# Optimization experiments

Hardware: AMD Instinct MI355X
Metric: run time of the kernel (lower is better)

The kernel has to match this reference:

```python
import jax, jax.numpy as jnp
import numpy as np

B, S, DIN, DOUT, R, E = 4, 4096, 2048, 2048, 16, 12
MULTIPLIER = 1.0
SCALE = 16.0 / 16.0  # alpha / lora_dim


def setup_inputs() -> dict:
    key = jax.random.key(0)
    k_x, k_g, k_org, k_dn, k_up = jax.random.split(key, 5)
    x = jax.random.normal(k_x, (B, S, DIN), dtype=jnp.float32)
    # router gate over experts (external router output; softmax-normalized)
    gate = jax.nn.softmax(jax.random.normal(k_g, (B, E), dtype=jnp.float32), axis=-1)
    W_org = jax.random.normal(k_org, (DOUT, DIN), dtype=jnp.float32) * (1.0 / np.sqrt(DIN))
    W_down = jax.random.normal(k_dn, (R, DIN), dtype=jnp.float32) * (1.0 / np.sqrt(DIN))
    W_up = jax.random.normal(k_up, (E, DOUT, R), dtype=jnp.float32) * 0.02
    return {"x": x, "gate": gate, "W_org": W_org, "W_down": W_down, "W_up": W_up}


def reference(x, gate, W_org, W_down, W_up):
    # Frozen base linear (no bias)
    org = jnp.einsum('bsi,oi->bso', x, W_org)
    # Shared down-projection to rank R
    lx = jnp.einsum('bsi,ri->bsr', x, W_down)                 # [B,S,R]
    # Gate-weighted combination of expert up-projections
    combined = jnp.einsum('be,eor->bor', gate, W_up)          # [B,DOUT,R]
    # Batched low-rank up-projection (torch bmm(lx, combined^T))
    out = jnp.einsum('bsr,bor->bso', lx, combined)            # [B,S,DOUT]
    return org + out * (MULTIPLIER * SCALE)
```

## Files before the change

### kernel.cpp

```cpp
#include <hip/hip_runtime.h>
#include <cstdint>
#include <cstddef>

#define B_    4
#define S_    4096
#define DIN_  2048
#define DOUT_ 2048
#define R_    16
#define E_    12

typedef __bf16 bf16x8  __attribute__((ext_vector_type(8)));
typedef float  floatx4  __attribute__((ext_vector_type(4)));
typedef float  floatx16 __attribute__((ext_vector_type(16)));

__device__ __forceinline__ unsigned int f2bf(float f) {
  unsigned int u = __builtin_bit_cast(unsigned int, f);
  u += 0x7fffu + ((u >> 16) & 1u);
  return u >> 16;
}

__device__ __forceinline__ void async_copy16(const void* g, void* l) {
  __builtin_amdgcn_global_load_lds(
      (const __attribute__((address_space(1))) void*)g,
      (__attribute__((address_space(3))) void*)l,
      16, 0, 0);
}

__global__ __launch_bounds__(256) void cvt_x_kernel(const float* __restrict__ x,
                                                    unsigned short* __restrict__ xb) {
  size_t idx = ((size_t)blockIdx.x * 256 + threadIdx.x) * 8;
  float4 a = *(const float4*)(x + idx);
  float4 b = *(const float4*)(x + idx + 4);
  uint4 o;
  o.x = f2bf(a.x) | (f2bf(a.y) << 16);
  o.y = f2bf(a.z) | (f2bf(a.w) << 16);
  o.z = f2bf(b.x) | (f2bf(b.y) << 16);
  o.w = f2bf(b.z) | (f2bf(b.w) << 16);
  *(uint4*)(xb + idx) = o;
}

__global__ __launch_bounds__(256) void prep_misc_kernel(const float* __restrict__ W_org,
                                                        const float* __restrict__ W_down,
                                                        const float* __restrict__ gate,
                                                        const float* __restrict__ W_up,
                                                        unsigned short* __restrict__ worg,
                                                        unsigned short* __restrict__ wdb,
                                                        unsigned short* __restrict__ cmb) {
  const int bid = blockIdx.x;
  const int tid = threadIdx.x;
  if (bid < 2064) {
    const float* src;
    unsigned short* dst;
    size_t idx;
    if (bid < 2048) { src = W_org;  dst = worg; idx = ((size_t)bid * 256 + tid) * 8; }
    else            { src = W_down; dst = wdb;  idx = ((size_t)(bid - 2048) * 256 + tid) * 8; }
    float4 a = *(const float4*)(src + idx);
    float4 b = *(const float4*)(src + idx + 4);
    uint4 o;
    o.x = f2bf(a.x) | (f2bf(a.y) << 16);
    o.y = f2bf(a.z) | (f2bf(a.w) << 16);
    o.z = f2bf(b.x) | (f2bf(b.y) << 16);
    o.w = f2bf(b.z) | (f2bf(b.w) << 16);
    *(uint4*)(dst + idx) = o;
  } else {
    const int idx = (bid - 2064) * 256 + tid;
    const int b   = idx >> 15;
    const int orr = idx & 32767;
    float s = 0.f;
#pragma unroll
    for (int e = 0; e < E_; ++e)
      s += gate[b * E_ + e] * W_up[(size_t)e * DOUT_ * R_ + orr];
    cmb[idx] = (unsigned short)f2bf(s);
  }
}

__global__ __launch_bounds__(256) void lx_kernel(const unsigned short* __restrict__ xb,
                                                 const unsigned short* __restrict__ wdb,
                                                 unsigned short* __restrict__ lxb) {
  const int tid  = threadIdx.x;
  const int lane = tid & 63;
  const int wave = tid >> 6;
  const int grp  = wave >> 1;
  const int kh   = wave & 1;
  const int q    = lane >> 4;
  const int mrow = lane & 15;
  const int row0 = blockIdx.x * 32 + grp * 16;

  floatx4 acc = {};
  const unsigned short* aptr = xb  + (size_t)(row0 + mrow) * DIN_ + kh * 1024 + q * 8;
  const unsigned short* bptr = wdb + (size_t)mrow * DIN_ + kh * 1024 + q * 8;
#pragma unroll 4
  for (int ks = 0; ks < 32; ++ks) {
    bf16x8 av = *(const bf16x8*)(aptr + ks * 32);
    bf16x8 bv = *(const bf16x8*)(bptr + ks * 32);
    acc = __builtin_amdgcn_mfma_f32_16x16x32_bf16(av, bv, acc, 0, 0, 0);
  }

  __shared__ float red[2][64 * 4];
  if (kh == 1) *(floatx4*)&red[grp][lane * 4] = acc;
  __syncthreads();
  if (kh == 0) {
    floatx4 o = *(const floatx4*)&red[grp][lane * 4];
    acc += o;
#pragma unroll
    for (int rg = 0; rg < 4; ++rg)
      lxb[(size_t)(row0 + q * 4 + rg) * R_ + mrow] = (unsigned short)f2bf(acc[rg]);
  }
}

__global__ __launch_bounds__(256) void gemm_kernel(const unsigned short* __restrict__ A,
                                                   const unsigned short* __restrict__ Bw,
                                                   const unsigned short* __restrict__ lx,
                                                   const unsigned short* __restrict__ cmb,
                                                   float* __restrict__ C) {
  constexpr int K = DIN_, N = DOUT_;
  __shared__ unsigned short lds[2 * 128 * 64];
  unsigned short* ldsA = lds;
  unsigned short* ldsB = lds + 128 * 64;

  const int tid  = threadIdx.x;
  const int lane = tid & 63;
  const int wave = tid >> 6;
  const int wm   = wave >> 1;
  const int wn   = wave & 1;
  const int g    = lane >> 5;
  const int mrow = lane & 31;

  const int mBase = blockIdx.y * 128;
  const int nBase = blockIdx.x * 128;
  const int batch = blockIdx.y >> 5;

  floatx16 acc[2][2] = {};

  for (int kt = 0; kt < K / 64; ++kt) {
    const int k0 = kt * 64;
#pragma unroll
    for (int is = 0; is < 4; ++is) {
      const int p    = is * 4096 + wave * 1024 + lane * 16;
      const int row  = p >> 7;
      const int slot = (p >> 4) & 7;
      const int ch   = slot ^ (row & 7);
      const unsigned short* ga = A  + (size_t)(mBase + row) * K + k0 + ch * 8;
      const unsigned short* gb = Bw + (size_t)(nBase + row) * K + k0 + ch * 8;
      async_copy16(ga, (char*)ldsA + p);
      async_copy16(gb, (char*)ldsB + p);
    }
    __syncthreads();

#pragma unroll
    for (int kc = 0; kc < 4; ++kc) {
      const int c = kc * 2 + g;
      bf16x8 af[2], bfr[2];
#pragma unroll
      for (int mt = 0; mt < 2; ++mt) {
        const int r = wm * 64 + mt * 32 + mrow;
        af[mt] = *(const bf16x8*)&ldsA[r * 64 + ((c ^ (r & 7)) << 3)];
      }
#pragma unroll
      for (int nt = 0; nt < 2; ++nt) {
        const int r = wn * 64 + nt * 32 + mrow;
        bfr[nt] = *(const bf16x8*)&ldsB[r * 64 + ((c ^ (r & 7)) << 3)];
      }
#pragma unroll
      for (int mt = 0; mt < 2; ++mt)
#pragma unroll
        for (int nt = 0; nt < 2; ++nt)
          acc[mt][nt] = __builtin_amdgcn_mfma_f32_32x32x16_bf16(af[mt], bfr[nt],
                                                                acc[mt][nt], 0, 0, 0);
    }
    __syncthreads();
  }

  {
    bf16x8 la[2], lb[2];
#pragma unroll
    for (int mt = 0; mt < 2; ++mt)
      la[mt] = *(const bf16x8*)&lx[(size_t)(mBase + wm * 64 + mt * 32 + mrow) * R_ + g * 8];
#pragma unroll
    for (int nt = 0; nt < 2; ++nt)
      lb[nt] = *(const bf16x8*)&cmb[((size_t)batch * DOUT_ + nBase + wn * 64 + nt * 32 + mrow) * R_ + g * 8];
#pragma unroll
    for (int mt = 0; mt < 2; ++mt)
#pragma unroll
      for (int nt = 0; nt < 2; ++nt)
        acc[mt][nt] = __builtin_amdgcn_mfma_f32_32x32x16_bf16(la[mt], lb[nt],
                                                              acc[mt][nt], 0, 0, 0);
  }

#pragma unroll
  for (int mt = 0; mt < 2; ++mt) {
#pragma unroll
    for (int nt = 0; nt < 2; ++nt) {
      const int gc  = nBase + wn * 64 + nt * 32 + mrow;
      const int gr0 = mBase + wm * 64 + mt * 32 + g * 4;
#pragma unroll
      for (int rg = 0; rg < 16; ++rg) {
        const int grow = gr0 + (rg & 3) + 8 * (rg >> 2);
        C[(size_t)grow * N + gc] = acc[mt][nt][rg];
      }
    }
  }
}

extern "C" void kernel_launch(void* const* d_in, const int* in_sizes, int n_in,
                              void* d_out, int out_size, void* d_ws, size_t ws_size,
                              hipStream_t stream) {
  const float* x      = (const float*)d_in[0];
  const float* gate   = (const float*)d_in[1];
  const float* W_org  = (const float*)d_in[2];
  const float* W_down = (const float*)d_in[3];
  const float* W_up   = (const float*)d_in[4];
  float* out = (float*)d_out;

  unsigned short* xb   = (unsigned short*)d_ws;
  unsigned short* worg = xb   + (size_t)B_ * S_ * DIN_;
  unsigned short* wdb  = worg + (size_t)DOUT_ * DIN_;
  unsigned short* lxb  = wdb  + (size_t)R_ * DIN_;
  unsigned short* cmb  = lxb  + (size_t)B_ * S_ * R_;

  cvt_x_kernel<<<(B_ * S_ * DIN_) / 2048, 256, 0, stream>>>(x, xb);

  prep_misc_kernel<<<2576, 256, 0, stream>>>(W_org, W_down, gate, W_up, worg, wdb, cmb);

  lx_kernel<<<(B_ * S_) / 32, 256, 0, stream>>>(xb, wdb, lxb);

  gemm_kernel<<<dim3(DOUT_ / 128, (B_ * S_) / 128), 256, 0, stream>>>(xb, worg, lxb, cmb, out);
}
```

Measured before the change: 396.3 us.

## Replace GEMM with 256x256 double-buffered, phase-pipelined MFMA kernel

Replaces the 128x128 single-buffered GEMM with a 512-thread kernel that computes 256x256 output tiles. It double-buffers the A and B tiles in LDS, staging the next K slice asynchronously while MFMA runs on the current one, and raises wave priority during compute. It also remaps block order so neighbouring blocks share tiles in cache. The LoRA correction now uses 16x16x32 MFMAs, with the unused K half zero-padded. The 128KB LDS buffer limits occupancy to one block per CU, and the larger accumulator set raises register pressure.

```diff
diff --git a/kernel.cpp b/kernel.cpp
--- a/kernel.cpp
+++ b/kernel.cpp
@@ -11,7 +11,6 @@
 
 typedef __bf16 bf16x8  __attribute__((ext_vector_type(8)));
 typedef float  floatx4  __attribute__((ext_vector_type(4)));
-typedef float  floatx16 __attribute__((ext_vector_type(16)));
 
 __device__ __forceinline__ unsigned int f2bf(float f) {
   unsigned int u = __builtin_bit_cast(unsigned int, f);
@@ -108,96 +107,135 @@
   }
 }
 
-__global__ __launch_bounds__(256) void gemm_kernel(const unsigned short* __restrict__ A,
-                                                   const unsigned short* __restrict__ Bw,
-                                                   const unsigned short* __restrict__ lx,
-                                                   const unsigned short* __restrict__ cmb,
-                                                   float* __restrict__ C) {
-  constexpr int K = DIN_, N = DOUT_;
-  __shared__ unsigned short lds[2 * 128 * 64];
-  unsigned short* ldsA = lds;
-  unsigned short* ldsB = lds + 128 * 64;
+__global__ __launch_bounds__(512, 2) void gemm256_kernel(const unsigned short* __restrict__ A,
+                                                         const unsigned short* __restrict__ Bw,
+                                                         const unsigned short* __restrict__ lx,
+                                                         const unsigned short* __restrict__ cmb,
+                                                         float* __restrict__ C) {
+  constexpr int K = DIN_;
+  __shared__ __align__(16) unsigned short lds[4 * 16384];
+  unsigned short* ldsA0 = lds;
+  unsigned short* ldsB0 = lds + 16384;
+  unsigned short* ldsA1 = lds + 32768;
+  unsigned short* ldsB1 = lds + 49152;
 
   const int tid  = threadIdx.x;
   const int lane = tid & 63;
   const int wave = tid >> 6;
-  const int wm   = wave >> 1;
-  const int wn   = wave & 1;
-  const int g    = lane >> 5;
-  const int mrow = lane & 31;
-
-  const int mBase = blockIdx.y * 128;
-  const int nBase = blockIdx.x * 128;
-  const int batch = blockIdx.y >> 5;
-
-  floatx16 acc[2][2] = {};
-
-  for (int kt = 0; kt < K / 64; ++kt) {
-    const int k0 = kt * 64;
-#pragma unroll
-    for (int is = 0; is < 4; ++is) {
-      const int p    = is * 4096 + wave * 1024 + lane * 16;
-      const int row  = p >> 7;
-      const int slot = (p >> 4) & 7;
-      const int ch   = slot ^ (row & 7);
-      const unsigned short* ga = A  + (size_t)(mBase + row) * K + k0 + ch * 8;
-      const unsigned short* gb = Bw + (size_t)(nBase + row) * K + k0 + ch * 8;
-      async_copy16(ga, (char*)ldsA + p);
-      async_copy16(gb, (char*)ldsB + p);
-    }
-    __syncthreads();
-
-#pragma unroll
-    for (int kc = 0; kc < 4; ++kc) {
-      const int c = kc * 2 + g;
-      bf16x8 af[2], bfr[2];
-#pragma unroll
-      for (int mt = 0; mt < 2; ++mt) {
-        const int r = wm * 64 + mt * 32 + mrow;
-        af[mt] = *(const bf16x8*)&ldsA[r * 64 + ((c ^ (r & 7)) << 3)];
-      }
-#pragma unroll
-      for (int nt = 0; nt < 2; ++nt) {
-        const int r = wn * 64 + nt * 32 + mrow;
-        bfr[nt] = *(const bf16x8*)&ldsB[r * 64 + ((c ^ (r & 7)) << 3)];
-      }
-#pragma unroll
-      for (int mt = 0; mt < 2; ++mt)
-#pragma unroll
-        for (int nt = 0; nt < 2; ++nt)
-          acc[mt][nt] = __builtin_amdgcn_mfma_f32_32x32x16_bf16(af[mt], bfr[nt],
-                                                                acc[mt][nt], 0, 0, 0);
-    }
-    __syncthreads();
-  }
+  const int wm   = wave >> 2;
+  const int wn   = wave & 3;
+  const int u    = lane & 15;
+  const int q    = lane >> 4;
+
+  const int lin = blockIdx.x;
+  const int swz = (lin & 7) * 64 + (lin >> 3);
+  const int by  = swz >> 3;
+  const int bx  = swz & 7;
+  const int mBase = by * 256;
+  const int nBase = bx * 256;
+  const int batch = by >> 4;
+
+  const int aBase = (wm * 128 + u) * 64;
+  const int bBase = (wn * 64 + u) * 64;
+  const int swzK0 = (q ^ (u & 7)) << 3;
+  const int swzK1 = ((4 + q) ^ (u & 7)) << 3;
+
+  floatx4 acc[8][4] = {};
+  bf16x8 af[4], bfv[4];
+
+  auto stage = [&](const unsigned short* __restrict__ src, unsigned short* dstBase,
+                   int rowBase, int k0) {
+#pragma unroll
+    for (int j = 0; j < 4; ++j) {
+      const int p   = j * 8192 + tid * 16;
+      const int row = p >> 7;
+      const int sp  = (p >> 4) & 7;
+      const int ss  = sp ^ (row & 7);
+      async_copy16(src + (size_t)(rowBase + row) * K + k0 + ss * 8,
+                   (char*)dstBase + p);
+    }
+  };
+
+  stage(A,  ldsA0, mBase, 0);
+  stage(Bw, ldsB0, nBase, 0);
+  asm volatile("s_waitcnt vmcnt(0)" ::: "memory");
+  __builtin_amdgcn_s_barrier();
+
+#define PHASE(h, SWZ, bufA, bufB, READB, STAGECODE, VMWAIT)                      \
+  {                                                                              \
+    _Pragma("unroll")                                                            \
+    for (int mf2 = 0; mf2 < 4; ++mf2)                                            \
+      af[mf2] = *(const bf16x8*)&bufA[aBase + ((h) * 4 + mf2) * 1024 + (SWZ)];   \
+    if (READB) {                                                                 \
+      _Pragma("unroll")                                                          \
+      for (int nf = 0; nf < 4; ++nf)                                             \
+        bfv[nf] = *(const bf16x8*)&bufB[bBase + nf * 1024 + (SWZ)];              \
+    }                                                                            \
+    STAGECODE;                                                                   \
+    __builtin_amdgcn_s_barrier();                                                \
+    asm volatile("s_waitcnt lgkmcnt(0)" ::: "memory");                           \
+    __builtin_amdgcn_s_setprio(1);                                               \
+    _Pragma("unroll")                                                            \
+    for (int mf2 = 0; mf2 < 4; ++mf2) {                                          \
+      _Pragma("unroll")                                                          \
+      for (int nf = 0; nf < 4; ++nf)                                             \
+        acc[(h) * 4 + mf2][nf] = __builtin_amdgcn_mfma_f32_16x16x32_bf16(        \
+            af[mf2], bfv[nf], acc[(h) * 4 + mf2][nf], 0, 0, 0);                  \
+    }                                                                            \
+    __builtin_amdgcn_s_setprio(0);                                               \
+    VMWAIT;                                                                      \
+    __builtin_amdgcn_s_barrier();                                                \
+  }
+
+  for (int it = 0; it < 16; ++it) {
+    const int kB = it * 128 + 64;
+    const int kN = it * 128 + 128;
+    const bool more = (it < 15);
+    PHASE(0, swzK0, ldsA0, ldsB0, true,  stage(A,  ldsA1, mBase, kB), )
+    PHASE(1, swzK0, ldsA0, ldsB0, false, stage(Bw, ldsB1, nBase, kB), )
+    PHASE(0, swzK1, ldsA0, ldsB0, true,  , )
+    PHASE(1, swzK1, ldsA0, ldsB0, false, ,
+          asm volatile("s_waitcnt vmcnt(0)" ::: "memory"))
+    PHASE(0, swzK0, ldsA1, ldsB1, true,  if (more) stage(A,  ldsA0, mBase, kN), )
+    PHASE(1, swzK0, ldsA1, ldsB1, false, if (more) stage(Bw, ldsB0, nBase, kN), )
+    PHASE(0, swzK1, ldsA1, ldsB1, true,  , )
+    PHASE(1, swzK1, ldsA1, ldsB1, false, ,
+          asm volatile("s_waitcnt vmcnt(0)" ::: "memory"))
+  }
+#undef PHASE
 
   {
-    bf16x8 la[2], lb[2];
-#pragma unroll
-    for (int mt = 0; mt < 2; ++mt)
-      la[mt] = *(const bf16x8*)&lx[(size_t)(mBase + wm * 64 + mt * 32 + mrow) * R_ + g * 8];
-#pragma unroll
-    for (int nt = 0; nt < 2; ++nt)
-      lb[nt] = *(const bf16x8*)&cmb[((size_t)batch * DOUT_ + nBase + wn * 64 + nt * 32 + mrow) * R_ + g * 8];
-#pragma unroll
-    for (int mt = 0; mt < 2; ++mt)
-#pragma unroll
-      for (int nt = 0; nt < 2; ++nt)
-        acc[mt][nt] = __builtin_amdgcn_mfma_f32_32x32x16_bf16(la[mt], lb[nt],
-                                                              acc[mt][nt], 0, 0, 0);
-  }
-
-#pragma unroll
-  for (int mt = 0; mt < 2; ++mt) {
-#pragma unroll
-    for (int nt = 0; nt < 2; ++nt) {
-      const int gc  = nBase + wn * 64 + nt * 32 + mrow;
-      const int gr0 = mBase + wm * 64 + mt * 32 + g * 4;
-#pragma unroll
-      for (int rg = 0; rg < 16; ++rg) {
-        const int grow = gr0 + (rg & 3) + 8 * (rg >> 2);
-        C[(size_t)grow * N + gc] = acc[mt][nt][rg];
-      }
+    bf16x8 z = {};
+    bf16x8 la[8], lb[4];
+#pragma unroll
+    for (int mf = 0; mf < 8; ++mf) {
+      const size_t row = (size_t)(mBase + wm * 128 + mf * 16 + u);
+      const unsigned short* p = lx + row * R_ + (q & 1) * 8;
+      la[mf] = (q < 2) ? *(const bf16x8*)p : z;
+    }
+#pragma unroll
+    for (int nf = 0; nf < 4; ++nf) {
+      const size_t brow = (size_t)batch * DOUT_ + nBase + wn * 64 + nf * 16 + u;
+      const unsigned short* p = cmb + brow * R_ + (q & 1) * 8;
+      lb[nf] = (q < 2) ? *(const bf16x8*)p : z;
+    }
+#pragma unroll
+    for (int mf = 0; mf < 8; ++mf)
+#pragma unroll
+      for (int nf = 0; nf < 4; ++nf)
+        acc[mf][nf] = __builtin_amdgcn_mfma_f32_16x16x32_bf16(la[mf], lb[nf],
+                                                              acc[mf][nf], 0, 0, 0);
+  }
+
+#pragma unroll
+  for (int mf = 0; mf < 8; ++mf) {
+    const int grow0 = mBase + wm * 128 + mf * 16 + q * 4;
+#pragma unroll
+    for (int nf = 0; nf < 4; ++nf) {
+      const int gcol = nBase + wn * 64 + nf * 16 + u;
+#pragma unroll
+      for (int rg = 0; rg < 4; ++rg)
+        C[(size_t)(grow0 + rg) * DOUT_ + gcol] = acc[mf][nf][rg];
     }
   }
 }
@@ -224,5 +262,5 @@
 
   lx_kernel<<<(B_ * S_) / 32, 256, 0, stream>>>(xb, wdb, lxb);
 
-  gemm_kernel<<<dim3(DOUT_ / 128, (B_ * S_) / 128), 256, 0, stream>>>(xb, worg, lxb, cmb, out);
-}
+  gemm256_kernel<<<512, 512, 0, stream>>>(xb, worg, lxb, cmb, out);
+}
```

Measured after the change: 372.3 us. -6.1%, faster.
